# Kernel optimization log

Measured on AMD Instinct MI355X. Metric: run time of the kernel, lower is better.

Reference implementation:

```python
import jax, jax.numpy as jnp
import numpy as np

N_NODES = 100000
N_EDGES = 1200000
D_IN = 16
D_EDGE = 4
H = 64


def setup_inputs() -> dict:
    key = jax.random.key(0)
    ks = jax.random.split(key, 20)
    s = 0.05
    inp = {
        "src": jax.random.randint(ks[0], (N_EDGES,), 0, N_NODES),
        "dst": jax.random.randint(ks[1], (N_EDGES,), 0, N_NODES),
        "t": jax.random.uniform(ks[2], (N_EDGES,), dtype=jnp.float32),
        "x": jax.random.normal(ks[3], (N_NODES, D_IN), dtype=jnp.float32),
        "edge_attr": jax.random.normal(ks[4], (N_EDGES, D_EDGE), dtype=jnp.float32),
        # x_encoder
        "Wx": jax.random.normal(ks[5], (D_IN, H), dtype=jnp.float32) * s,
        "bx": jnp.zeros((H,), dtype=jnp.float32),
        # TransformerConv (heads=1, concat=False)
        "Wq": jax.random.normal(ks[6], (H, H), dtype=jnp.float32) * s,
        "bq": jnp.zeros((H,), dtype=jnp.float32),
        "Wk": jax.random.normal(ks[7], (H, H), dtype=jnp.float32) * s,
        "bk": jnp.zeros((H,), dtype=jnp.float32),
        "Wv": jax.random.normal(ks[8], (H, H), dtype=jnp.float32) * s,
        "bv": jnp.zeros((H,), dtype=jnp.float32),
        "We": jax.random.normal(ks[9], (D_EDGE, H), dtype=jnp.float32) * s,  # lin_edge, bias=False
        "Ws": jax.random.normal(ks[10], (H, H), dtype=jnp.float32) * s,  # lin_skip (root weight)
        "bs": jnp.zeros((H,), dtype=jnp.float32),
        # MLP head
        "W1": jax.random.normal(ks[11], (H, 8), dtype=jnp.float32) * s,
        "b1": jnp.zeros((8,), dtype=jnp.float32),
        "W2": jax.random.normal(ks[12], (8, 1), dtype=jnp.float32) * s,
        "b2": jnp.zeros((1,), dtype=jnp.float32),
    }
    return inp


def reference(src, dst, t, x, edge_attr, Wx, bx, Wq, bq, Wk, bk, Wv, bv, We, Ws, bs, W1, b1, W2, b2):
    # eval mode: dropouts are identity; TGN memory.update_state is a pure
    # side effect and does not influence the returned output.
    xe = x @ Wx + bx                             # [N, H]

    # TransformerConv, heads=1, concat=False, flow src -> dst
    q = xe @ Wq + bq                             # [N, H]
    k = xe @ Wk + bk                             # [N, H]
    v = xe @ Wv + bv                             # [N, H]
    e = edge_attr @ We                           # [E, H]

    k_e = k[src] + e                             # [E, H]
    v_e = v[src] + e                             # [E, H]
    alpha = jnp.sum(q[dst] * k_e, axis=-1) / jnp.sqrt(jnp.float32(H))  # [E]

    # softmax over incoming edges per destination node
    m = jax.ops.segment_max(alpha, dst, num_segments=N_NODES)
    a = jnp.exp(alpha - m[dst])
    denom = jax.ops.segment_sum(a, dst, num_segments=N_NODES)
    w = a / (denom[dst] + 1e-16)                 # [E]

    agg = jax.ops.segment_sum(v_e * w[:, None], dst, num_segments=N_NODES)  # [N, H]
    h_local = agg + (xe @ Ws + bs)               # root/skip connection

    h = h_local[dst]                             # [E, H]
    h = jax.nn.relu(h @ W1 + b1)                 # [E, 8]
    out = (h @ W2 + b2)[:, 0]                    # [E]
    return out
```

## Files before the change

### kernel.cpp

```cpp
#include <hip/hip_runtime.h>

#define OFF_M   0
#define OFF_U   256
#define OFF_W   272
#define OFF_C   288
#define OFF_R   292
#define OFF_R0  356
#define OFF_PV  360
#define OFF_PE  488
#define OFF_PS  520
#define OFF_BH1 648
#define OFF_BH2 656
#define CST_N   664

#define NB      64
#define CAPB    1152
#define CHB     8192
#define MAXBUCK 2048

typedef int nint4 __attribute__((ext_vector_type(4)));

__device__ __forceinline__ unsigned f2bf(float f) {
    unsigned u = __float_as_uint(f);
    u += 0x7fffu + ((u >> 16) & 1u);
    return u >> 16;
}
__device__ __forceinline__ float bf_lo(unsigned u) { return __uint_as_float(u << 16); }
__device__ __forceinline__ float bf_hi(unsigned u) { return __uint_as_float(u & 0xffff0000u); }

struct Params {
    const int* src; const int* dst; const float4* ea4; const float* x;
    const float* Wx; const float* bx;
    const float* Wq; const float* bq;
    const float* Wk; const float* bk;
    const float* Wv; const float* bv;
    const float* We; const float* Ws; const float* bs;
    const float* W1; const float* b1; const float* W2; const float* b2;
    float* cst;
    float* srec;
    float* drec;
    float* xps;
    float* g;
    nint4* recs;
    int* gcur;
    float* out;
    int N, E;
};

__device__ void do_fold(const Params& P, float* __restrict__ cst)
{
    __shared__ float sWf[4][16][64];
    __shared__ float sbf[4][64];
    const int t = threadIdx.x;
    const int c = t & 63, m = t >> 6;
    const float* W; const float* b;
    switch (m) {
        case 0:  W = P.Wq; b = P.bq; break;
        case 1:  W = P.Wk; b = P.bk; break;
        case 2:  W = P.Wv; b = P.bv; break;
        default: W = P.Ws; b = P.bs; break;
    }
    float acc[16];
#pragma unroll
    for (int i = 0; i < 16; ++i) acc[i] = 0.f;
    float bacc = b[c];
#pragma unroll 8
    for (int j = 0; j < 64; ++j) {
        const float wv = W[j * 64 + c];
        bacc += P.bx[j] * wv;
#pragma unroll
        for (int i = 0; i < 16; ++i) acc[i] += P.Wx[i * 64 + j] * wv;
    }
#pragma unroll
    for (int i = 0; i < 16; ++i) sWf[m][i][c] = acc[i];
    sbf[m][c] = bacc;
    __syncthreads();

    {
        const int i = t >> 4, j = t & 15;
        float s = 0.f;
#pragma unroll 8
        for (int cc = 0; cc < 64; ++cc) s += sWf[0][i][cc] * sWf[1][j][cc];
        cst[OFF_M + i * 16 + j] = s;
    }
    if (t < 16) {
        float su = 0.f, sw = 0.f;
#pragma unroll 8
        for (int cc = 0; cc < 64; ++cc) {
            su += sWf[1][t][cc] * sbf[0][cc];
            sw += sWf[0][t][cc] * sbf[1][cc];
        }
        cst[OFF_U + t] = su;
        cst[OFF_W + t] = sw;
    }
    if (t == 0) {
        float s = 0.f;
#pragma unroll 8
        for (int cc = 0; cc < 64; ++cc) s += sbf[0][cc] * sbf[1][cc];
        cst[OFF_C] = s;
    }
    if (t < 64) {
        const int j = t >> 4, i = t & 15;
        float s = 0.f;
#pragma unroll 8
        for (int cc = 0; cc < 64; ++cc) s += P.We[j * 64 + cc] * sWf[0][i][cc];
        cst[OFF_R + j * 16 + i] = s;
    }
    if (t < 4) {
        float s = 0.f;
#pragma unroll 8
        for (int cc = 0; cc < 64; ++cc) s += P.We[t * 64 + cc] * sbf[0][cc];
        cst[OFF_R0 + t] = s;
    }
    if (t < 128) {
        const int i = t >> 3, j = t & 7;
        float sv = 0.f, ss = 0.f;
#pragma unroll 8
        for (int cc = 0; cc < 64; ++cc) {
            const float w1 = P.W1[cc * 8 + j];
            sv += sWf[2][i][cc] * w1;
            ss += sWf[3][i][cc] * w1;
        }
        cst[OFF_PV + i * 8 + j] = sv;
        cst[OFF_PS + i * 8 + j] = ss;
    }
    if (t < 32) {
        const int mm = t >> 3, j = t & 7;
        float s = 0.f;
#pragma unroll 8
        for (int cc = 0; cc < 64; ++cc) s += P.We[mm * 64 + cc] * P.W1[cc * 8 + j];
        cst[OFF_PE + mm * 8 + j] = s;
    }
    if (t < 8) {
        float s1 = 0.f, s2 = 0.f;
#pragma unroll 8
        for (int cc = 0; cc < 64; ++cc) {
            const float w1 = P.W1[cc * 8 + t];
            s1 += sbf[2][cc] * w1;
            s2 += sbf[3][cc] * w1;
        }
        cst[OFF_BH1 + t] = s1;
        cst[OFF_BH2 + t] = s2 + P.b1[t];
    }
}

__global__ __launch_bounds__(256) void k_init(Params P)
{
    if (blockIdx.x == 0) { do_fold(P, P.cst); return; }
    const int nbuck = (P.N + NB - 1) >> 6;
    const int i = ((int)blockIdx.x - 1) * 256 + threadIdx.x;
    if (i < nbuck) P.gcur[i] = 0;
}

__global__ __launch_bounds__(256) void k_node(Params P)
{
    __shared__ float sx[16][16];
    const float* __restrict__ cst = P.cst;
    const int t = threadIdx.x;
    const int node0 = blockIdx.x * 16;
    const int nl = t >> 4, cg = t & 15;
    {
        const int idx = node0 * 16 + t;
        sx[nl][cg] = (idx < P.N * 16) ? P.x[idx] : 0.f;
    }
    __syncthreads();
    const int n = node0 + nl;
    if (n >= P.N) return;

    float y = cst[OFF_U + cg];
#pragma unroll
    for (int i = 0; i < 16; ++i)
        y += sx[nl][i] * cst[OFF_M + i * 16 + cg];

    const float xv = sx[nl][cg];
    const float yp = __shfl_xor(y, 1);
    const float xp = __shfl_xor(xv, 1);
    if ((cg & 1) == 0) {
        ((unsigned*)P.drec)[(size_t)n * 16 + (cg >> 1)] = f2bf(y) | (f2bf(yp) << 16);
        ((unsigned*)P.srec)[(size_t)n * 16 + (cg >> 1)] = f2bf(xv) | (f2bf(xp) << 16);
    }

    if (cg < 8) {
        float s = 0.f;
#pragma unroll
        for (int i = 0; i < 16; ++i)
            s += sx[nl][i] * cst[OFF_PV + i * 8 + cg];
        P.srec[(size_t)n * 16 + 8 + cg] = s;
    } else {
        const int j = cg - 8;
        float s = 0.f;
#pragma unroll
        for (int i = 0; i < 16; ++i)
            s += sx[nl][i] * cst[OFF_PS + i * 8 + j];
        P.xps[(size_t)n * 8 + j] = s;
    }
    if (cg < 4) {
        float r = cst[OFF_R0 + cg];
#pragma unroll
        for (int i = 0; i < 16; ++i)
            r += cst[OFF_R + cg * 16 + i] * sx[nl][i];
        P.drec[(size_t)n * 16 + 8 + cg] = r;
    }
}

__global__ __launch_bounds__(512) void k_bin(Params P)
{
    __shared__ int lh[MAXBUCK];
    const int t = threadIdx.x;
    const int nbuck = (P.N + NB - 1) >> 6;
    for (int b = t; b < nbuck; b += 512) lh[b] = 0;
    __syncthreads();

    const int e0 = blockIdx.x * CHB;
    const int nval = min(CHB, P.E - e0);
    int dreg[16];
#pragma unroll
    for (int k = 0; k < 16; ++k) {
        const int o = t + k * 512;
        dreg[k] = (o < nval) ? P.dst[e0 + o] : -1;
    }
#pragma unroll
    for (int k = 0; k < 16; ++k)
        if (dreg[k] >= 0) atomicAdd(&lh[dreg[k] >> 6], 1);
    __syncthreads();

    for (int b = t; b < nbuck; b += 512) {
        const int c = lh[b];
        lh[b] = c ? atomicAdd(&P.gcur[b], c) : 0;
    }
    __syncthreads();

#pragma unroll
    for (int k = 0; k < 16; ++k) {
        const int d = dreg[k];
        if (d < 0) continue;
        const int e = e0 + t + k * 512;
        const int bb = d >> 6;
        const int pos = atomicAdd(&lh[bb], 1);
        if (pos < CAPB) {
            const float4 A = P.ea4[e];
            nint4 r;
            r.x = P.src[e];
            r.y = d & (NB - 1);
            r.z = (int)(f2bf(A.x) | (f2bf(A.y) << 16));
            r.w = (int)(f2bf(A.z) | (f2bf(A.w) << 16));
            P.recs[(size_t)bb * CAPB + pos] = r;
        }
    }
}

__global__ __launch_bounds__(256) void k_agg(Params P)
{
    __shared__ unsigned sdy[NB * 8];
    __shared__ float sdrv[NB * 4];
    __shared__ float sacc[NB * 10];
    const int t = threadIdx.x;
    const int b = blockIdx.x;
    const int n0 = b << 6;
    const float* __restrict__ cst = P.cst;

    const unsigned* dr = (const unsigned*)P.drec + (size_t)n0 * 16;
    for (int i = t; i < NB * 16; i += 256) {
        const int m = i >> 4, j = i & 15;
        const unsigned w = dr[i];
        if (j < 8) sdy[m * 8 + j] = w;
        else if (j < 12) sdrv[m * 4 + (j - 8)] = __uint_as_float(w);
    }
    for (int i = t; i < NB * 10; i += 256) sacc[i] = 0.f;
    __syncthreads();

    const int cnt = min(P.gcur[b], CAPB);
    const int G = t >> 3;
    const int cg = t & 7;
    const float pe0 = cst[OFF_PE + 0 * 8 + cg];
    const float pe1 = cst[OFF_PE + 1 * 8 + cg];
    const float pe2 = cst[OFF_PE + 2 * 8 + cg];
    const float pe3 = cst[OFF_PE + 3 * 8 + cg];
    const nint4* __restrict__ rb = P.recs + (size_t)b * CAPB;
    const unsigned* __restrict__ sr = (const unsigned*)P.srec;

    if (G < cnt) {
        const int iB0 = G + 32;
        nint4 rA = rb[G];
        nint4 rB = rb[iB0 < cnt ? iB0 : G];
        unsigned xwA = sr[(size_t)rA.x * 16 + cg];
        float pvsA = __uint_as_float(sr[(size_t)rA.x * 16 + 8 + cg]);

        for (int i = G; i < cnt; i += 32) {
            const int iC = i + 64;
            const nint4 rC = rb[iC < cnt ? iC : i];
            const unsigned xwB = sr[(size_t)rB.x * 16 + cg];
            const float pvsB = __uint_as_float(sr[(size_t)rB.x * 16 + 8 + cg]);

            const int dl = rA.y;
            const float A0 = bf_lo((unsigned)rA.z), A1 = bf_hi((unsigned)rA.z);
            const float A2 = bf_lo((unsigned)rA.w), A3 = bf_hi((unsigned)rA.w);
            const unsigned yw = sdy[dl * 8 + cg];

            float p = bf_lo(xwA) * bf_lo(yw) + bf_hi(xwA) * bf_hi(yw);
            p += __shfl_xor(p, 1);
            p += __shfl_xor(p, 2);
            p += __shfl_xor(p, 4);
            p += A0 * sdrv[dl * 4 + 0] + A1 * sdrv[dl * 4 + 1]
               + A2 * sdrv[dl * 4 + 2] + A3 * sdrv[dl * 4 + 3];
            const float a = __expf(p * 0.125f);

            atomicAdd(&sacc[dl * 10 + cg],
                      a * (pvsA + A0 * pe0 + A1 * pe1 + A2 * pe2 + A3 * pe3));
            if (cg == 0) atomicAdd(&sacc[dl * 10 + 8], a);

            rA = rB; rB = rC; xwA = xwB; pvsA = pvsB;
        }
    }
    __syncthreads();

    if (t < NB) {
        const int n = n0 + t;
        if (n < P.N) {
            const float den = sacc[t * 10 + 8];
            const float inv = 1.f / (den + 1e-16f);
            const float dinv = den * inv;
            float val = P.b2[0];
#pragma unroll
            for (int j = 0; j < 8; ++j) {
                const float hid = inv * sacc[t * 10 + j]
                                + P.xps[(size_t)n * 8 + j]
                                + dinv * cst[OFF_BH1 + j] + cst[OFF_BH2 + j];
                val += fmaxf(hid, 0.f) * P.W2[j];
            }
            P.g[n] = val;
        }
    }
}

__global__ __launch_bounds__(256) void k_out(
    const int* __restrict__ dst, const float* __restrict__ g,
    float* __restrict__ out, int E)
{
    const int e = blockIdx.x * 256 + threadIdx.x;
    if (e < E) out[e] = g[dst[e]];
}

extern "C" void kernel_launch(void* const* d_in, const int* in_sizes, int n_in,
                              void* d_out, int out_size, void* d_ws, size_t ws_size,
                              hipStream_t stream)
{
    Params P;
    P.src = (const int*)d_in[0];
    P.dst = (const int*)d_in[1];
    P.x   = (const float*)d_in[3];
    P.ea4 = (const float4*)d_in[4];
    P.Wx  = (const float*)d_in[5];
    P.bx  = (const float*)d_in[6];
    P.Wq  = (const float*)d_in[7];
    P.bq  = (const float*)d_in[8];
    P.Wk  = (const float*)d_in[9];
    P.bk  = (const float*)d_in[10];
    P.Wv  = (const float*)d_in[11];
    P.bv  = (const float*)d_in[12];
    P.We  = (const float*)d_in[13];
    P.Ws  = (const float*)d_in[14];
    P.bs  = (const float*)d_in[15];
    P.W1  = (const float*)d_in[16];
    P.b1  = (const float*)d_in[17];
    P.W2  = (const float*)d_in[18];
    P.b2  = (const float*)d_in[19];

    P.E = in_sizes[0];
    P.N = in_sizes[3] / 16;
    P.out = (float*)d_out;

    const int nbuck = (P.N + NB - 1) >> 6;

    float* w = (float*)d_ws;
    P.recs = (nint4*)w;   w += (size_t)nbuck * CAPB * 4;
    P.srec = w;           w += (size_t)P.N * 16;
    P.drec = w;           w += (size_t)P.N * 16;
    P.xps  = w;           w += (size_t)P.N * 8;
    P.g    = w;           w += (size_t)P.N;
    P.gcur = (int*)w;     w += nbuck;
    P.cst  = w;

    const int nbE = (P.E + 255) / 256;

    k_init<<<1 + (nbuck + 255) / 256, 256, 0, stream>>>(P);
    k_node<<<(P.N + 15) / 16, 256, 0, stream>>>(P);
    k_bin<<<(P.E + CHB - 1) / CHB, 512, 0, stream>>>(P);
    k_agg<<<nbuck, 256, 0, stream>>>(P);
    k_out<<<nbE, 256, 0, stream>>>(P.dst, P.g, P.out, P.E);
}
```

Measured before the change: 257.0 us.

## Interleave source record fields and batch four edges per group with shuffled record loads

The source-node record now interleaves the packed bf16 feature word and its projected value, so one 8-byte load fetches both instead of two separate 4-byte loads. The aggregation loop has each 8-lane group load four edge records cooperatively, with one int2 per lane, and distribute them by shuffles. It then issues four independent gathers before computing, replacing the previous software-pipelined one-edge-at-a-time loop. The aim is more memory-level parallelism and fewer, wider loads, at the cost of extra shuffles and predication on partial batches.

```diff
diff --git a/kernel.cpp b/kernel.cpp
--- a/kernel.cpp
+++ b/kernel.cpp
@@ -177,7 +177,7 @@
     const float xp = __shfl_xor(xv, 1);
     if ((cg & 1) == 0) {
         ((unsigned*)P.drec)[(size_t)n * 16 + (cg >> 1)] = f2bf(y) | (f2bf(yp) << 16);
-        ((unsigned*)P.srec)[(size_t)n * 16 + (cg >> 1)] = f2bf(xv) | (f2bf(xp) << 16);
+        ((unsigned*)P.srec)[(size_t)n * 16 + cg] = f2bf(xv) | (f2bf(xp) << 16);
     }
 
     if (cg < 8) {
@@ -185,7 +185,7 @@
 #pragma unroll
         for (int i = 0; i < 16; ++i)
             s += sx[nl][i] * cst[OFF_PV + i * 8 + cg];
-        P.srec[(size_t)n * 16 + 8 + cg] = s;
+        P.srec[(size_t)n * 16 + 2 * cg + 1] = s;
     } else {
         const int j = cg - 8;
         float s = 0.f;
@@ -272,32 +272,48 @@
     const int cnt = min(P.gcur[b], CAPB);
     const int G = t >> 3;
     const int cg = t & 7;
+    const int base = (t & 63) & 56;
     const float pe0 = cst[OFF_PE + 0 * 8 + cg];
     const float pe1 = cst[OFF_PE + 1 * 8 + cg];
     const float pe2 = cst[OFF_PE + 2 * 8 + cg];
     const float pe3 = cst[OFF_PE + 3 * 8 + cg];
-    const nint4* __restrict__ rb = P.recs + (size_t)b * CAPB;
-    const unsigned* __restrict__ sr = (const unsigned*)P.srec;
-
-    if (G < cnt) {
-        const int iB0 = G + 32;
-        nint4 rA = rb[G];
-        nint4 rB = rb[iB0 < cnt ? iB0 : G];
-        unsigned xwA = sr[(size_t)rA.x * 16 + cg];
-        float pvsA = __uint_as_float(sr[(size_t)rA.x * 16 + 8 + cg]);
-
-        for (int i = G; i < cnt; i += 32) {
-            const int iC = i + 64;
-            const nint4 rC = rb[iC < cnt ? iC : i];
-            const unsigned xwB = sr[(size_t)rB.x * 16 + cg];
-            const float pvsB = __uint_as_float(sr[(size_t)rB.x * 16 + 8 + cg]);
-
-            const int dl = rA.y;
-            const float A0 = bf_lo((unsigned)rA.z), A1 = bf_hi((unsigned)rA.z);
-            const float A2 = bf_lo((unsigned)rA.w), A3 = bf_hi((unsigned)rA.w);
+    const int2* __restrict__ rb2 = (const int2*)(P.recs + (size_t)b * CAPB);
+    const int2* __restrict__ sr2 = (const int2*)P.srec;
+
+    for (int i0 = G * 4; i0 < cnt; i0 += 128) {
+        const int2 rl = rb2[(size_t)i0 * 2 + cg];
+
+        int  sA[4], dlA[4];
+        unsigned a01[4], a23[4];
+#pragma unroll
+        for (int k = 0; k < 4; ++k) {
+            sA[k]  = __shfl(rl.x, base + 2 * k);
+            dlA[k] = __shfl(rl.y, base + 2 * k) & (NB - 1);
+            a01[k] = (unsigned)__shfl(rl.x, base + 2 * k + 1);
+            a23[k] = (unsigned)__shfl(rl.y, base + 2 * k + 1);
+        }
+
+        int2 sv0, sv1, sv2, sv3;
+        {
+            const bool v1 = (i0 + 1) < cnt, v2 = (i0 + 2) < cnt, v3 = (i0 + 3) < cnt;
+            sv0 = sr2[(size_t)sA[0] * 8 + cg];
+            sv1 = sr2[(size_t)(v1 ? sA[1] : 0) * 8 + cg];
+            sv2 = sr2[(size_t)(v2 ? sA[2] : 0) * 8 + cg];
+            sv3 = sr2[(size_t)(v3 ? sA[3] : 0) * 8 + cg];
+        }
+
+#pragma unroll
+        for (int k = 0; k < 4; ++k) {
+            const bool v = (i0 + k) < cnt;
+            const int dl = dlA[k];
+            const int2 sv = (k == 0) ? sv0 : (k == 1) ? sv1 : (k == 2) ? sv2 : sv3;
+            const float A0 = bf_lo(a01[k]), A1 = bf_hi(a01[k]);
+            const float A2 = bf_lo(a23[k]), A3 = bf_hi(a23[k]);
+            const unsigned xw = (unsigned)sv.x;
+            const float pvs = __int_as_float(sv.y);
             const unsigned yw = sdy[dl * 8 + cg];
 
-            float p = bf_lo(xwA) * bf_lo(yw) + bf_hi(xwA) * bf_hi(yw);
+            float p = bf_lo(xw) * bf_lo(yw) + bf_hi(xw) * bf_hi(yw);
             p += __shfl_xor(p, 1);
             p += __shfl_xor(p, 2);
             p += __shfl_xor(p, 4);
@@ -305,11 +321,11 @@
                + A2 * sdrv[dl * 4 + 2] + A3 * sdrv[dl * 4 + 3];
             const float a = __expf(p * 0.125f);
 
-            atomicAdd(&sacc[dl * 10 + cg],
-                      a * (pvsA + A0 * pe0 + A1 * pe1 + A2 * pe2 + A3 * pe3));
-            if (cg == 0) atomicAdd(&sacc[dl * 10 + 8], a);
-
-            rA = rB; rB = rC; xwA = xwB; pvsA = pvsB;
+            if (v) {
+                atomicAdd(&sacc[dl * 10 + cg],
+                          a * (pvs + A0 * pe0 + A1 * pe1 + A2 * pe2 + A3 * pe3));
+                if (cg == 0) atomicAdd(&sacc[dl * 10 + 8], a);
+            }
         }
     }
     __syncthreads();
```

After: 270.7 us. 1.05x slower.

## Split each aggregation bucket across two blocks with global atomic accumulation

Applied to the files above, without the earlier changes.

Each destination bucket's edge list is now processed by two blocks, each taking alternate 32-edge strides. The blocks merge their shared-memory partial sums into a new global accumulator with atomics, and a new k_fin kernel applies the MLP head. The binning chunk also shrinks so k_bin launches more blocks, and the software prefetch pipeline in the aggregation loop is removed. This raises parallelism and occupancy for the latency-bound aggregation, at the cost of an extra launch, global atomics, zeroing the accumulator in k_node, and a redundant shared-memory preload per half.

```diff
diff --git a/kernel.cpp b/kernel.cpp
--- a/kernel.cpp
+++ b/kernel.cpp
@@ -15,7 +15,7 @@
 
 #define NB      64
 #define CAPB    1152
-#define CHB     8192
+#define CHB     4096
 #define MAXBUCK 2048
 
 typedef int nint4 __attribute__((ext_vector_type(4)));
@@ -39,6 +39,7 @@
     float* cst;
     float* srec;
     float* drec;
+    float* acc;
     float* xps;
     float* g;
     nint4* recs;
@@ -201,6 +202,7 @@
             r += cst[OFF_R + cg * 16 + i] * sx[nl][i];
         P.drec[(size_t)n * 16 + 8 + cg] = r;
     }
+    P.acc[(size_t)n * 16 + cg] = 0.f;
 }
 
 __global__ __launch_bounds__(512) void k_bin(Params P)
@@ -213,14 +215,14 @@
 
     const int e0 = blockIdx.x * CHB;
     const int nval = min(CHB, P.E - e0);
-    int dreg[16];
-#pragma unroll
-    for (int k = 0; k < 16; ++k) {
+    int dreg[8];
+#pragma unroll
+    for (int k = 0; k < 8; ++k) {
         const int o = t + k * 512;
         dreg[k] = (o < nval) ? P.dst[e0 + o] : -1;
     }
 #pragma unroll
-    for (int k = 0; k < 16; ++k)
+    for (int k = 0; k < 8; ++k)
         if (dreg[k] >= 0) atomicAdd(&lh[dreg[k] >> 6], 1);
     __syncthreads();
 
@@ -231,7 +233,7 @@
     __syncthreads();
 
 #pragma unroll
-    for (int k = 0; k < 16; ++k) {
+    for (int k = 0; k < 8; ++k) {
         const int d = dreg[k];
         if (d < 0) continue;
         const int e = e0 + t + k * 512;
@@ -255,7 +257,8 @@
     __shared__ float sdrv[NB * 4];
     __shared__ float sacc[NB * 10];
     const int t = threadIdx.x;
-    const int b = blockIdx.x;
+    const int b = blockIdx.x >> 1;
+    const int half = blockIdx.x & 1;
     const int n0 = b << 6;
     const float* __restrict__ cst = P.cst;
 
@@ -279,58 +282,55 @@
     const nint4* __restrict__ rb = P.recs + (size_t)b * CAPB;
     const unsigned* __restrict__ sr = (const unsigned*)P.srec;
 
-    if (G < cnt) {
-        const int iB0 = G + 32;
-        nint4 rA = rb[G];
-        nint4 rB = rb[iB0 < cnt ? iB0 : G];
-        unsigned xwA = sr[(size_t)rA.x * 16 + cg];
-        float pvsA = __uint_as_float(sr[(size_t)rA.x * 16 + 8 + cg]);
-
-        for (int i = G; i < cnt; i += 32) {
-            const int iC = i + 64;
-            const nint4 rC = rb[iC < cnt ? iC : i];
-            const unsigned xwB = sr[(size_t)rB.x * 16 + cg];
-            const float pvsB = __uint_as_float(sr[(size_t)rB.x * 16 + 8 + cg]);
-
-            const int dl = rA.y;
-            const float A0 = bf_lo((unsigned)rA.z), A1 = bf_hi((unsigned)rA.z);
-            const float A2 = bf_lo((unsigned)rA.w), A3 = bf_hi((unsigned)rA.w);
-            const unsigned yw = sdy[dl * 8 + cg];
-
-            float p = bf_lo(xwA) * bf_lo(yw) + bf_hi(xwA) * bf_hi(yw);
-            p += __shfl_xor(p, 1);
-            p += __shfl_xor(p, 2);
-            p += __shfl_xor(p, 4);
-            p += A0 * sdrv[dl * 4 + 0] + A1 * sdrv[dl * 4 + 1]
-               + A2 * sdrv[dl * 4 + 2] + A3 * sdrv[dl * 4 + 3];
-            const float a = __expf(p * 0.125f);
-
-            atomicAdd(&sacc[dl * 10 + cg],
-                      a * (pvsA + A0 * pe0 + A1 * pe1 + A2 * pe2 + A3 * pe3));
-            if (cg == 0) atomicAdd(&sacc[dl * 10 + 8], a);
-
-            rA = rB; rB = rC; xwA = xwB; pvsA = pvsB;
-        }
-    }
-    __syncthreads();
-
-    if (t < NB) {
-        const int n = n0 + t;
-        if (n < P.N) {
-            const float den = sacc[t * 10 + 8];
-            const float inv = 1.f / (den + 1e-16f);
-            const float dinv = den * inv;
-            float val = P.b2[0];
-#pragma unroll
-            for (int j = 0; j < 8; ++j) {
-                const float hid = inv * sacc[t * 10 + j]
-                                + P.xps[(size_t)n * 8 + j]
-                                + dinv * cst[OFF_BH1 + j] + cst[OFF_BH2 + j];
-                val += fmaxf(hid, 0.f) * P.W2[j];
-            }
-            P.g[n] = val;
-        }
-    }
+    for (int i = G + (half << 5); i < cnt; i += 64) {
+        const nint4 r = rb[i];
+        const int s = r.x, dl = r.y;
+        const float A0 = bf_lo((unsigned)r.z), A1 = bf_hi((unsigned)r.z);
+        const float A2 = bf_lo((unsigned)r.w), A3 = bf_hi((unsigned)r.w);
+        const unsigned xw = sr[(size_t)s * 16 + cg];
+        const float pvs = __uint_as_float(sr[(size_t)s * 16 + 8 + cg]);
+        const unsigned yw = sdy[dl * 8 + cg];
+
+        float p = bf_lo(xw) * bf_lo(yw) + bf_hi(xw) * bf_hi(yw);
+        p += __shfl_xor(p, 1);
+        p += __shfl_xor(p, 2);
+        p += __shfl_xor(p, 4);
+        p += A0 * sdrv[dl * 4 + 0] + A1 * sdrv[dl * 4 + 1]
+           + A2 * sdrv[dl * 4 + 2] + A3 * sdrv[dl * 4 + 3];
+        const float a = __expf(p * 0.125f);
+
+        atomicAdd(&sacc[dl * 10 + cg],
+                  a * (pvs + A0 * pe0 + A1 * pe1 + A2 * pe2 + A3 * pe3));
+        if (cg == 0) atomicAdd(&sacc[dl * 10 + 8], a);
+    }
+    __syncthreads();
+
+    for (int i = t; i < NB * 9; i += 256) {
+        const int nl = i / 9, j = i - nl * 9;
+        const int n = n0 + nl;
+        if (n < P.N)
+            atomicAdd(&P.acc[(size_t)n * 16 + j], sacc[nl * 10 + j]);
+    }
+}
+
+__global__ __launch_bounds__(256) void k_fin(Params P)
+{
+    const int n = blockIdx.x * 256 + threadIdx.x;
+    if (n >= P.N) return;
+    const float* __restrict__ cst = P.cst;
+    const float* accn = &P.acc[(size_t)n * 16];
+    const float den = accn[8];
+    const float inv = 1.f / (den + 1e-16f);
+    const float dinv = den * inv;
+    float val = P.b2[0];
+#pragma unroll
+    for (int j = 0; j < 8; ++j) {
+        const float hid = inv * accn[j]
+                        + P.xps[(size_t)n * 8 + j]
+                        + dinv * cst[OFF_BH1 + j] + cst[OFF_BH2 + j];
+        val += fmaxf(hid, 0.f) * P.W2[j];
+    }
+    P.g[n] = val;
 }
 
 __global__ __launch_bounds__(256) void k_out(
@@ -376,6 +376,7 @@
     P.recs = (nint4*)w;   w += (size_t)nbuck * CAPB * 4;
     P.srec = w;           w += (size_t)P.N * 16;
     P.drec = w;           w += (size_t)P.N * 16;
+    P.acc  = w;           w += (size_t)P.N * 16;
     P.xps  = w;           w += (size_t)P.N * 8;
     P.g    = w;           w += (size_t)P.N;
     P.gcur = (int*)w;     w += nbuck;
@@ -386,6 +387,7 @@
     k_init<<<1 + (nbuck + 255) / 256, 256, 0, stream>>>(P);
     k_node<<<(P.N + 15) / 16, 256, 0, stream>>>(P);
     k_bin<<<(P.E + CHB - 1) / CHB, 512, 0, stream>>>(P);
-    k_agg<<<nbuck, 256, 0, stream>>>(P);
+    k_agg<<<nbuck * 2, 256, 0, stream>>>(P);
+    k_fin<<<(P.N + 255) / 256, 256, 0, stream>>>(P);
     k_out<<<nbE, 256, 0, stream>>>(P.dst, P.g, P.out, P.E);
 }
```

Result: slower. 269.2 us (+4.7%).

## Aggregate raw source features per node and apply value projection after reduction

Applied to the files above, without the earlier changes.

Instead of gathering a precomputed 8-wide projected value vector per source node, the aggregation kernel accumulates attention-weighted raw bf16 source features (16) and edge attributes (4) in shared memory. The linear value/edge projection is applied once per destination node in the epilogue. This halves the per-node source record to 32 bytes, cutting gather traffic, and removes the software-pipelined prefetch of records. In exchange it roughly doubles shared atomics per edge and adds a small per-node matvec in the epilogue.

```diff
diff --git a/kernel.cpp b/kernel.cpp
--- a/kernel.cpp
+++ b/kernel.cpp
@@ -177,22 +177,15 @@
     const float xp = __shfl_xor(xv, 1);
     if ((cg & 1) == 0) {
         ((unsigned*)P.drec)[(size_t)n * 16 + (cg >> 1)] = f2bf(y) | (f2bf(yp) << 16);
-        ((unsigned*)P.srec)[(size_t)n * 16 + (cg >> 1)] = f2bf(xv) | (f2bf(xp) << 16);
+        ((unsigned*)P.srec)[(size_t)n * 8 + (cg >> 1)] = f2bf(xv) | (f2bf(xp) << 16);
     }
 
     if (cg < 8) {
         float s = 0.f;
 #pragma unroll
         for (int i = 0; i < 16; ++i)
-            s += sx[nl][i] * cst[OFF_PV + i * 8 + cg];
-        P.srec[(size_t)n * 16 + 8 + cg] = s;
-    } else {
-        const int j = cg - 8;
-        float s = 0.f;
-#pragma unroll
-        for (int i = 0; i < 16; ++i)
-            s += sx[nl][i] * cst[OFF_PS + i * 8 + j];
-        P.xps[(size_t)n * 8 + j] = s;
+            s += sx[nl][i] * cst[OFF_PS + i * 8 + cg];
+        P.xps[(size_t)n * 8 + cg] = s;
     }
     if (cg < 4) {
         float r = cst[OFF_R0 + cg];
@@ -253,7 +246,7 @@
 {
     __shared__ unsigned sdy[NB * 8];
     __shared__ float sdrv[NB * 4];
-    __shared__ float sacc[NB * 10];
+    __shared__ float sacc[NB * 24];
     const int t = threadIdx.x;
     const int b = blockIdx.x;
     const int n0 = b << 6;
@@ -266,50 +259,38 @@
         if (j < 8) sdy[m * 8 + j] = w;
         else if (j < 12) sdrv[m * 4 + (j - 8)] = __uint_as_float(w);
     }
-    for (int i = t; i < NB * 10; i += 256) sacc[i] = 0.f;
+    for (int i = t; i < NB * 24; i += 256) sacc[i] = 0.f;
     __syncthreads();
 
     const int cnt = min(P.gcur[b], CAPB);
     const int G = t >> 3;
     const int cg = t & 7;
-    const float pe0 = cst[OFF_PE + 0 * 8 + cg];
-    const float pe1 = cst[OFF_PE + 1 * 8 + cg];
-    const float pe2 = cst[OFF_PE + 2 * 8 + cg];
-    const float pe3 = cst[OFF_PE + 3 * 8 + cg];
     const nint4* __restrict__ rb = P.recs + (size_t)b * CAPB;
-    const unsigned* __restrict__ sr = (const unsigned*)P.srec;
-
-    if (G < cnt) {
-        const int iB0 = G + 32;
-        nint4 rA = rb[G];
-        nint4 rB = rb[iB0 < cnt ? iB0 : G];
-        unsigned xwA = sr[(size_t)rA.x * 16 + cg];
-        float pvsA = __uint_as_float(sr[(size_t)rA.x * 16 + 8 + cg]);
-
-        for (int i = G; i < cnt; i += 32) {
-            const int iC = i + 64;
-            const nint4 rC = rb[iC < cnt ? iC : i];
-            const unsigned xwB = sr[(size_t)rB.x * 16 + cg];
-            const float pvsB = __uint_as_float(sr[(size_t)rB.x * 16 + 8 + cg]);
-
-            const int dl = rA.y;
-            const float A0 = bf_lo((unsigned)rA.z), A1 = bf_hi((unsigned)rA.z);
-            const float A2 = bf_lo((unsigned)rA.w), A3 = bf_hi((unsigned)rA.w);
-            const unsigned yw = sdy[dl * 8 + cg];
-
-            float p = bf_lo(xwA) * bf_lo(yw) + bf_hi(xwA) * bf_hi(yw);
-            p += __shfl_xor(p, 1);
-            p += __shfl_xor(p, 2);
-            p += __shfl_xor(p, 4);
-            p += A0 * sdrv[dl * 4 + 0] + A1 * sdrv[dl * 4 + 1]
-               + A2 * sdrv[dl * 4 + 2] + A3 * sdrv[dl * 4 + 3];
-            const float a = __expf(p * 0.125f);
-
-            atomicAdd(&sacc[dl * 10 + cg],
-                      a * (pvsA + A0 * pe0 + A1 * pe1 + A2 * pe2 + A3 * pe3));
-            if (cg == 0) atomicAdd(&sacc[dl * 10 + 8], a);
-
-            rA = rB; rB = rC; xwA = xwB; pvsA = pvsB;
+    const unsigned* __restrict__ sr8 = (const unsigned*)P.srec;
+
+    for (int i = G; i < cnt; i += 32) {
+        const nint4 r = rb[i];
+        const int s = r.x, dl = r.y;
+        const float A0 = bf_lo((unsigned)r.z), A1 = bf_hi((unsigned)r.z);
+        const float A2 = bf_lo((unsigned)r.w), A3 = bf_hi((unsigned)r.w);
+        const unsigned xw = sr8[(size_t)s * 8 + cg];
+        const unsigned yw = sdy[dl * 8 + cg];
+
+        float p = bf_lo(xw) * bf_lo(yw) + bf_hi(xw) * bf_hi(yw);
+        p += __shfl_xor(p, 1);
+        p += __shfl_xor(p, 2);
+        p += __shfl_xor(p, 4);
+        p += A0 * sdrv[dl * 4 + 0] + A1 * sdrv[dl * 4 + 1]
+           + A2 * sdrv[dl * 4 + 2] + A3 * sdrv[dl * 4 + 3];
+        const float a = __expf(p * 0.125f);
+
+        atomicAdd(&sacc[dl * 24 + 2 * cg],     a * bf_lo(xw));
+        atomicAdd(&sacc[dl * 24 + 2 * cg + 1], a * bf_hi(xw));
+        if (cg < 4) {
+            const float Am = cg == 0 ? A0 : cg == 1 ? A1 : cg == 2 ? A2 : A3;
+            atomicAdd(&sacc[dl * 24 + 16 + cg], a * Am);
+        } else if (cg == 4) {
+            atomicAdd(&sacc[dl * 24 + 20], a);
         }
     }
     __syncthreads();
@@ -317,13 +298,24 @@
     if (t < NB) {
         const int n = n0 + t;
         if (n < P.N) {
-            const float den = sacc[t * 10 + 8];
+            float T[16];
+#pragma unroll
+            for (int i = 0; i < 16; ++i) T[i] = sacc[t * 24 + i];
+            float S[4];
+#pragma unroll
+            for (int m = 0; m < 4; ++m) S[m] = sacc[t * 24 + 16 + m];
+            const float den = sacc[t * 24 + 20];
             const float inv = 1.f / (den + 1e-16f);
             const float dinv = den * inv;
             float val = P.b2[0];
 #pragma unroll
             for (int j = 0; j < 8; ++j) {
-                const float hid = inv * sacc[t * 10 + j]
+                float h = 0.f;
+#pragma unroll
+                for (int i = 0; i < 16; ++i) h += T[i] * cst[OFF_PV + i * 8 + j];
+#pragma unroll
+                for (int m = 0; m < 4; ++m) h += S[m] * cst[OFF_PE + m * 8 + j];
+                const float hid = h * inv
                                 + P.xps[(size_t)n * 8 + j]
                                 + dinv * cst[OFF_BH1 + j] + cst[OFF_BH2 + j];
                 val += fmaxf(hid, 0.f) * P.W2[j];
@@ -374,7 +366,7 @@
 
     float* w = (float*)d_ws;
     P.recs = (nint4*)w;   w += (size_t)nbuck * CAPB * 4;
-    P.srec = w;           w += (size_t)P.N * 16;
+    P.srec = w;           w += (size_t)P.N * 8;
     P.drec = w;           w += (size_t)P.N * 16;
     P.xps  = w;           w += (size_t)P.N * 8;
     P.g    = w;           w += (size_t)P.N;
```

After: 350.2 us. 36.2% more time.
